# Kernel optimization log

Measured on AMD Instinct MI355X. Metric: run time of the kernel, lower is better.

Reference implementation:

```python
import jax, jax.numpy as jnp
import numpy as np

D_MODEL = 1024
N_HEADS = 16
SEQ = 2048
BATCH = 2
EPS = 1e-5


def layer_norm(x, g, b):
    mu = jnp.mean(x, axis=-1, keepdims=True)
    var = jnp.mean(jnp.square(x - mu), axis=-1, keepdims=True)
    return (x - mu) * jax.lax.rsqrt(var + EPS) * g + b


def setup_inputs() -> dict:
    key = jax.random.key(0)
    ks = jax.random.split(key, 10)
    D = D_MODEL
    s = lambda fan_in: 1.0 / np.sqrt(fan_in)
    return {
        "x": jax.random.normal(ks[0], (BATCH, SEQ, D), dtype=jnp.float32),
        # weights stored [in, out] (torch Linear is y = x @ W.T; equivalent math)
        "w_attn": jax.random.uniform(ks[1], (D, 3 * D), minval=-s(D), maxval=s(D), dtype=jnp.float32),
        "b_attn": jnp.zeros((3 * D,), jnp.float32),
        "w_proj": jax.random.uniform(ks[2], (D, D), minval=-s(D), maxval=s(D), dtype=jnp.float32),
        "b_proj": jnp.zeros((D,), jnp.float32),
        "ln1_g": jnp.ones((D,), jnp.float32),
        "ln1_b": jnp.zeros((D,), jnp.float32),
        "ln2_g": jnp.ones((D,), jnp.float32),
        "ln2_b": jnp.zeros((D,), jnp.float32),
        "w_fc1": jax.random.uniform(ks[3], (D, 4 * D), minval=-s(D), maxval=s(D), dtype=jnp.float32),
        "b_fc1": jnp.zeros((4 * D,), jnp.float32),
        "w_fc2": jax.random.uniform(ks[4], (4 * D, D), minval=-s(4 * D), maxval=s(4 * D), dtype=jnp.float32),
        "b_fc2": jnp.zeros((D,), jnp.float32),
    }


def reference(x, w_attn, b_attn, w_proj, b_proj, ln1_g, ln1_b, ln2_g, ln2_b, w_fc1, b_fc1, w_fc2, b_fc2):
    B, L, D = x.shape
    H = N_HEADS
    Dh = D // H

    # --- attention sublayer ---
    h = layer_norm(x, ln1_g, ln1_b)
    qkv = h @ w_attn + b_attn                      # [B, L, 3D]
    # SOURCE BUG (faithful): q, k, v are all taken from the k third.
    k = qkv[..., D:2 * D]
    kh = k.reshape(B, L, H, Dh).transpose(0, 2, 1, 3)   # [B, H, L, Dh]
    att = jnp.einsum('bhqd,bhkd->bhqk', kh, kh) / jnp.sqrt(jnp.float32(Dh))
    att = jax.nn.softmax(att, axis=-1)
    out = jnp.einsum('bhqk,bhkd->bhqd', att, kh)         # [B, H, L, Dh]
    out = out.transpose(0, 2, 1, 3).reshape(B, L, D)
    x = x + (out @ w_proj + b_proj)

    # --- feed-forward sublayer ---
    h = layer_norm(x, ln2_g, ln2_b)
    h = jax.nn.relu(h @ w_fc1 + b_fc1)
    x = x + (h @ w_fc2 + b_fc2)
    return x
```

## Files before the change

### kernel.cpp

```cpp
#include <hip/hip_runtime.h>


typedef __attribute__((ext_vector_type(8))) short s8v;
typedef __attribute__((ext_vector_type(4))) short s4v;
typedef __attribute__((ext_vector_type(4))) float f4v;

#define D_MODEL 1024
#define SEQ 2048
#define BATCH 2
#define NH 16
#define DH 64
#define MROWS (BATCH * SEQ)

#define KH_SCALE 0.42466088f
#define KH_ISCALE 2.3548200f

__device__ __forceinline__ float b2f(unsigned short u) {
  union { unsigned int i; float f; } v; v.i = ((unsigned int)u) << 16; return v.f;
}
__device__ __forceinline__ unsigned short f2b(float f) {
  unsigned int i = __builtin_bit_cast(unsigned int, f);
  unsigned int r = (i + 0x7fffu + ((i >> 16) & 1u)) >> 16;
  return (unsigned short)r;
}
__device__ __forceinline__ void async16(const void* g, void* l) {
  __builtin_amdgcn_global_load_lds(
      (const __attribute__((address_space(1))) unsigned int*)g,
      (__attribute__((address_space(3))) unsigned int*)l, 16, 0, 0);
}
__device__ __forceinline__ unsigned short cvt_b(float f) { return f2b(f); }
__device__ __forceinline__ unsigned short cvt_b(unsigned short u) { return u; }

__device__ __forceinline__ float xp2(float x) {
#if __has_builtin(__builtin_amdgcn_exp2f)
  return __builtin_amdgcn_exp2f(x);
#else
  return exp2f(x);
#endif
}

__device__ __forceinline__ s4v cvt4(float a, float b, float c, float d) {
  unsigned int lo, hi;
  asm("v_cvt_pk_bf16_f32 %0, %1, %2" : "=v"(lo) : "v"(a), "v"(b));
  asm("v_cvt_pk_bf16_f32 %0, %1, %2" : "=v"(hi) : "v"(c), "v"(d));
  union { unsigned long long u; s4v v; } u;
  u.u = ((unsigned long long)hi << 32) | (unsigned long long)lo;
  return u.v;
}

#if __has_builtin(__builtin_amdgcn_mfma_f32_16x16x16_bf16)
__device__ __forceinline__ f4v mfma16(s4v a, s4v b, f4v c) {
  return __builtin_amdgcn_mfma_f32_16x16x16_bf16(a, b, c, 0, 0, 0);
}
#elif __has_builtin(__builtin_amdgcn_mfma_f32_16x16x16bf16_1k)
__device__ __forceinline__ f4v mfma16(s4v a, s4v b, f4v c) {
  return __builtin_amdgcn_mfma_f32_16x16x16bf16_1k(a, b, c, 0, 0, 0);
}
#else
__device__ __forceinline__ f4v mfma16(s4v a, s4v b, f4v c) {
  s8v aa = {a[0], a[1], a[2], a[3], 0, 0, 0, 0};
  s8v bb = {b[0], b[1], b[2], b[3], 0, 0, 0, 0};
  return __builtin_amdgcn_mfma_f32_16x16x32_bf16(aa, bb, c, 0, 0, 0);
}
#endif

__global__ __launch_bounds__(256) void ln_kernel(
    const float* __restrict__ x, const float* __restrict__ g,
    const float* __restrict__ bb, unsigned short* __restrict__ out) {
  int row = blockIdx.x;
  int t = threadIdx.x;
  const float* xr = x + (size_t)row * D_MODEL;
  float v[4];
  float s = 0.f, s2 = 0.f;
#pragma unroll
  for (int i = 0; i < 4; ++i) {
    float f = xr[t + 256 * i];
    v[i] = f; s += f; s2 += f * f;
  }
#pragma unroll
  for (int off = 1; off < 64; off <<= 1) {
    s += __shfl_xor(s, off, 64);
    s2 += __shfl_xor(s2, off, 64);
  }
  __shared__ float red[8];
  if ((t & 63) == 0) { red[t >> 6] = s; red[4 + (t >> 6)] = s2; }
  __syncthreads();
  s = red[0] + red[1] + red[2] + red[3];
  s2 = red[4] + red[5] + red[6] + red[7];
  float mu = s * (1.f / D_MODEL);
  float var = s2 * (1.f / D_MODEL) - mu * mu;
  float rstd = rsqrtf(var + 1e-5f);
#pragma unroll
  for (int i = 0; i < 4; ++i) {
    int c = t + 256 * i;
    float h = (v[i] - mu) * rstd * g[c] + bb[c];
    out[(size_t)row * D_MODEL + c] = f2b(h);
  }
}

template <typename T>
__global__ __launch_bounds__(256) void transpose_b(
    const T* __restrict__ src, unsigned short* __restrict__ dst,
    int srcStride, int dstStride, long long srcBatch, long long dstBatch) {
  __shared__ unsigned short tile[64][65];
  const T* s = src + (size_t)blockIdx.z * srcBatch;
  unsigned short* d = dst + (size_t)blockIdx.z * dstBatch;
  int n0 = blockIdx.x * 64, k0 = blockIdx.y * 64;
  for (int i = threadIdx.x; i < 4096; i += 256) {
    int k = i >> 6, n = i & 63;
    tile[k][n] = cvt_b(s[(size_t)(k0 + k) * srcStride + n0 + n]);
  }
  __syncthreads();
  for (int i = threadIdx.x; i < 4096; i += 256) {
    int n = i >> 6, k = i & 63;
    d[(size_t)(n0 + n) * dstStride + k0 + k] = tile[k][n];
  }
}

template <int RES, bool RELU, bool KH, int OUTF, int BN>
__global__ __launch_bounds__(256) void gemm_bt(
    const unsigned short* __restrict__ A, const unsigned short* __restrict__ Bt,
    const float* __restrict__ bias, const float* __restrict__ res,
    void* __restrict__ out, int M, int N, int K) {
  constexpr int NT = BN / 32;
  __shared__ __align__(16) unsigned short lsA[128 * 64];
  __shared__ __align__(16) unsigned short lsB[BN * 64];
  int tid = threadIdx.x;
  int lane = tid & 63, w = tid >> 6, quad = lane >> 4, l16 = lane & 15;
  int m0 = blockIdx.y * 128, n0 = blockIdx.x * BN;
  int wm = (w >> 1) * 64, wn = (w & 1) * (BN / 2);
  f4v acc[4][NT] = {};
  for (int kt = 0; kt < K; kt += 64) {
#pragma unroll
    for (int i = 0; i < 4; ++i) {
      int cb = w * 256 + i * 64;
      int ci = cb + lane;
      int row = ci >> 3, c = ci & 7;
      int cs = c ^ (row & 7);
      async16(A + (size_t)(m0 + row) * K + kt + cs * 8, &lsA[cb * 8]);
    }
#pragma unroll
    for (int i = 0; i < BN / 32; ++i) {
      int cb = w * (BN * 2) + i * 64;
      int ci = cb + lane;
      int row = ci >> 3, c = ci & 7;
      int cs = c ^ (row & 7);
      async16(Bt + (size_t)(n0 + row) * K + kt + cs * 8, &lsB[cb * 8]);
    }
    __builtin_amdgcn_s_waitcnt(0x0f70);
    __syncthreads();
#pragma unroll
    for (int s = 0; s < 2; ++s) {
      s8v af[4], bf[NT];
#pragma unroll
      for (int t = 0; t < 4; ++t) {
        int am = wm + t * 16 + l16;
        int ac = (s * 4 + quad) ^ (am & 7);
        af[t] = *(const s8v*)(&lsA[am * 64 + ac * 8]);
      }
#pragma unroll
      for (int t = 0; t < NT; ++t) {
        int bn = wn + t * 16 + l16;
        int bc = (s * 4 + quad) ^ (bn & 7);
        bf[t] = *(const s8v*)(&lsB[bn * 64 + bc * 8]);
      }
#pragma unroll
      for (int ti = 0; ti < 4; ++ti)
#pragma unroll
        for (int tj = 0; tj < NT; ++tj)
          acc[ti][tj] = __builtin_amdgcn_mfma_f32_16x16x32_bf16(
              af[ti], bf[tj], acc[ti][tj], 0, 0, 0);
    }
    __syncthreads();
  }
#pragma unroll
  for (int tj = 0; tj < NT; ++tj) {
    int col = n0 + wn + tj * 16 + l16;
    float bv = bias[col];
#pragma unroll
    for (int ti = 0; ti < 4; ++ti) {
#pragma unroll
      for (int r = 0; r < 4; ++r) {
        int rowg = m0 + wm + ti * 16 + quad * 4 + r;
        float vv = acc[ti][tj][r] + bv;
        if (KH) vv *= KH_SCALE;
        if (RES == 2) vv += res[(size_t)rowg * N + col];
        if (RELU) vv = fmaxf(vv, 0.f);
        size_t oidx;
        if (KH) {
          int b = rowg >> 11, l = rowg & 2047, h = col >> 6, d = col & 63;
          oidx = (((size_t)(b * NH + h)) * SEQ + l) * DH + d;
        } else {
          oidx = (size_t)rowg * N + col;
        }
        if (OUTF == 0) ((unsigned short*)out)[oidx] = f2b(vv);
        else           ((float*)out)[oidx] = vv;
      }
    }
  }
}

__global__ __launch_bounds__(256) void flash_k(
    const unsigned short* __restrict__ kh, const unsigned short* __restrict__ khT,
    unsigned short* __restrict__ Opart, float* __restrict__ lpart) {
  __shared__ __align__(16) unsigned short lsK[128 * 64];
  __shared__ __align__(16) unsigned short lsKT[64 * 128];
  int tid = threadIdx.x;
  int lane = tid & 63, w = tid >> 6, quad = lane >> 4, l16 = lane & 15;
  int split = blockIdx.x, bh = blockIdx.y, qb = blockIdx.z;
  const unsigned short* khB = kh + (size_t)bh * SEQ * DH;
  const unsigned short* khTB = khT + (size_t)bh * DH * SEQ;
  unsigned short* Op = Opart + (size_t)split * MROWS * D_MODEL;
  float* lp = lpart + (size_t)split * BATCH * NH * SEQ;
  s8v aQ[2][2];
#pragma unroll
  for (int g = 0; g < 2; ++g) {
    int q = qb * 128 + w * 32 + g * 16 + l16;
#pragma unroll
    for (int s = 0; s < 2; ++s)
      aQ[g][s] = *(const s8v*)(khB + (size_t)q * DH + s * 32 + quad * 8);
  }
  const s4v vone = {(short)0x3F80, (short)0x3F80, (short)0x3F80, (short)0x3F80};
  f4v accO[2][4] = {};
  f4v accL[2] = {};

  for (int kt8 = 0; kt8 < 8; ++kt8) {
    int key0 = split * 1024 + kt8 * 128;
#pragma unroll
    for (int i = 0; i < 4; ++i) {
      int cb = w * 256 + i * 64;
      int ci = cb + lane;
      int row = ci >> 3, c = ci & 7;
      int cs = c ^ (row & 7);
      async16(khB + (size_t)(key0 + row) * DH + cs * 8, &lsK[cb * 8]);
    }
#pragma unroll
    for (int i = 0; i < 4; ++i) {
      int cb = w * 256 + i * 64;
      int ci = cb + lane;
      int row = ci >> 4, c = ci & 15;
      int cs = c ^ (row & 15);
      async16(khTB + (size_t)row * SEQ + key0 + cs * 8, &lsKT[cb * 8]);
    }
    __builtin_amdgcn_s_waitcnt(0x0f70);
    __syncthreads();
#pragma unroll
    for (int half = 0; half < 2; ++half) {
      f4v accST[2][4] = {};
#pragma unroll
      for (int s = 0; s < 2; ++s) {
#pragma unroll
        for (int tj = 0; tj < 4; ++tj) {
          int key = half * 64 + tj * 16 + l16;
          int c = (s * 4 + quad) ^ (key & 7);
          s8v kf = *(const s8v*)(&lsK[key * 64 + c * 8]);
#pragma unroll
          for (int g = 0; g < 2; ++g)
            accST[g][tj] = __builtin_amdgcn_mfma_f32_16x16x32_bf16(
                kf, aQ[g][s], accST[g][tj], 0, 0, 0);
        }
      }
#pragma unroll
      for (int tj = 0; tj < 4; ++tj) {
        s4v pf[2];
#pragma unroll
        for (int g = 0; g < 2; ++g) {
          float p0 = xp2(accST[g][tj][0]);
          float p1 = xp2(accST[g][tj][1]);
          float p2 = xp2(accST[g][tj][2]);
          float p3 = xp2(accST[g][tj][3]);
          pf[g] = cvt4(p0, p1, p2, p3);
          accL[g] = mfma16(pf[g], vone, accL[g]);
        }
#pragma unroll
        for (int db = 0; db < 4; ++db) {
          int d = db * 16 + l16;
          int ch = (half * 8 + tj * 2 + (quad >> 1)) ^ (d & 15);
          s4v vf = *(const s4v*)(&lsKT[d * 128 + ch * 8 + (quad & 1) * 4]);
#pragma unroll
          for (int g = 0; g < 2; ++g)
            accO[g][db] = mfma16(pf[g], vf, accO[g][db]);
        }
      }
    }
    __syncthreads();
  }
  int b = bh >> 4, h = bh & 15;
#pragma unroll
  for (int g = 0; g < 2; ++g) {
    if (l16 == 0) {
#pragma unroll
      for (int r = 0; r < 4; ++r) {
        int q = qb * 128 + w * 32 + g * 16 + quad * 4 + r;
        lp[(size_t)bh * SEQ + q] = accL[g][r];
      }
    }
#pragma unroll
    for (int r = 0; r < 4; ++r) {
      int l = qb * 128 + w * 32 + g * 16 + quad * 4 + r;
#pragma unroll
      for (int db = 0; db < 4; ++db) {
        int d = db * 16 + l16;
        Op[((size_t)(b * SEQ + l)) * D_MODEL + h * DH + d] = f2b(accO[g][db][r]);
      }
    }
  }
}

__global__ __launch_bounds__(256) void attn_combine(
    const unsigned short* __restrict__ Opart, const float* __restrict__ lpart,
    unsigned short* __restrict__ attn) {
  int row = blockIdx.x;
  int b = row >> 11, l = row & 2047;
  int c0 = threadIdx.x * 4;
  int h = c0 >> 6;
  size_t lidx = (size_t)(b * NH + h) * SEQ + l;
  float ls = lpart[lidx] + lpart[(size_t)BATCH * NH * SEQ + lidx];
  float inv = KH_ISCALE / ls;
  s4v o0 = *(const s4v*)(Opart + (size_t)row * D_MODEL + c0);
  s4v o1 = *(const s4v*)(Opart + (size_t)MROWS * D_MODEL +
                         (size_t)row * D_MODEL + c0);
  s4v ov;
#pragma unroll
  for (int i = 0; i < 4; ++i)
    ov[i] = (short)f2b((b2f((unsigned short)o0[i]) +
                        b2f((unsigned short)o1[i])) * inv);
  *(s4v*)(attn + (size_t)row * D_MODEL + c0) = ov;
}

extern "C" void kernel_launch(void* const* d_in, const int* in_sizes, int n_in,
                              void* d_out, int out_size, void* d_ws, size_t ws_size,
                              hipStream_t stream) {
  (void)in_sizes; (void)n_in; (void)out_size;
  const float* x      = (const float*)d_in[0];
  const float* w_attn = (const float*)d_in[1];
  const float* b_attn = (const float*)d_in[2];
  const float* w_proj = (const float*)d_in[3];
  const float* b_proj = (const float*)d_in[4];
  const float* ln1_g  = (const float*)d_in[5];
  const float* ln1_b  = (const float*)d_in[6];
  const float* ln2_g  = (const float*)d_in[7];
  const float* ln2_b  = (const float*)d_in[8];
  const float* w_fc1  = (const float*)d_in[9];
  const float* b_fc1  = (const float*)d_in[10];
  const float* w_fc2  = (const float*)d_in[11];
  const float* b_fc2  = (const float*)d_in[12];

  char* ws = (char*)d_ws;
  float*          x1    = (float*)(ws);
  unsigned short* hbuf  = (unsigned short*)(ws + (size_t)(16u << 20));
  unsigned short* wT1   = (unsigned short*)(ws + (size_t)(24u << 20));
  unsigned short* wT2   = (unsigned short*)(ws + (size_t)(32u << 20));
  unsigned short* kh    = (unsigned short*)(ws + (size_t)(40u << 20));
  unsigned short* khT   = (unsigned short*)(ws + (size_t)(48u << 20));
  unsigned short* Opart = (unsigned short*)(ws);
  float*          lpart = (float*)(ws + (size_t)(16u << 20));
  unsigned short* fc1o  = kh;
  unsigned short* attn  = (unsigned short*)d_out;
  float* outf = (float*)d_out;
  bool big_ws = ws_size >= ((size_t)72u << 20);

  dim3 blk(256);
  hipLaunchKernelGGL(ln_kernel, dim3(MROWS), blk, 0, stream, x, ln1_g, ln1_b, hbuf);
  hipLaunchKernelGGL(transpose_b<float>, dim3(16, 16, 1), blk, 0, stream,
                     w_attn + 1024, wT1, 3 * D_MODEL, D_MODEL, 0LL, 0LL);
  hipLaunchKernelGGL((gemm_bt<0, false, true, 0, 64>), dim3(16, 32), blk, 0, stream,
                     hbuf, wT1, b_attn + 1024, nullptr, (void*)kh,
                     MROWS, D_MODEL, D_MODEL);
  hipLaunchKernelGGL(transpose_b<unsigned short>, dim3(1, 32, 32), blk, 0, stream,
                     kh, khT, DH, SEQ, (long long)(SEQ * DH), (long long)(DH * SEQ));
  hipLaunchKernelGGL(flash_k, dim3(2, 32, SEQ / 128), blk, 0, stream,
                     kh, khT, Opart, lpart);
  hipLaunchKernelGGL(attn_combine, dim3(MROWS), blk, 0, stream,
                     Opart, lpart, attn);
  hipLaunchKernelGGL(transpose_b<float>, dim3(16, 16, 1), blk, 0, stream,
                     w_proj, wT1, D_MODEL, D_MODEL, 0LL, 0LL);
  hipLaunchKernelGGL((gemm_bt<2, false, false, 1, 64>), dim3(16, 32), blk, 0, stream,
                     attn, wT1, b_proj, x, (void*)x1, MROWS, D_MODEL, D_MODEL);
  hipLaunchKernelGGL(ln_kernel, dim3(MROWS), blk, 0, stream, x1, ln2_g, ln2_b, hbuf);
  hipLaunchKernelGGL(transpose_b<float>, dim3(64, 16, 1), blk, 0, stream,
                     w_fc1, wT1, 4 * D_MODEL, D_MODEL, 0LL, 0LL);
  hipLaunchKernelGGL(transpose_b<float>, dim3(16, 64, 1), blk, 0, stream,
                     w_fc2, wT2, D_MODEL, 4 * D_MODEL, 0LL, 0LL);
  if (big_ws) {
    hipLaunchKernelGGL((gemm_bt<0, true, false, 0, 128>), dim3(32, 32), blk, 0, stream,
                       hbuf, wT1, b_fc1, nullptr, (void*)fc1o,
                       MROWS, 4 * D_MODEL, D_MODEL);
    hipLaunchKernelGGL((gemm_bt<2, false, false, 1, 64>), dim3(16, 32), blk, 0, stream,
                       fc1o, wT2, b_fc2, x1, (void*)outf,
                       MROWS, D_MODEL, 4 * D_MODEL);
  } else {
    for (int c = 0; c < 2; ++c) {
      const unsigned short* h2c = hbuf + (size_t)c * 2048 * D_MODEL;
      const float* x1c = x1 + (size_t)c * 2048 * D_MODEL;
      float* outc = outf + (size_t)c * 2048 * D_MODEL;
      hipLaunchKernelGGL((gemm_bt<0, true, false, 0, 128>), dim3(32, 16), blk, 0, stream,
                         h2c, wT1, b_fc1, nullptr, (void*)fc1o,
                         2048, 4 * D_MODEL, D_MODEL);
      hipLaunchKernelGGL((gemm_bt<2, false, false, 1, 64>), dim3(16, 16), blk, 0, stream,
                         fc1o, wT2, b_fc2, x1c, (void*)outc,
                         2048, D_MODEL, 4 * D_MODEL);
    }
  }
}
```

Measured before the change: 346.9 us.

## Double-buffer GEMM LDS tiles to overlap global loads with MFMA

The bf16 GEMM now keeps two LDS buffers for the A and B tiles. It issues the async loads for the next K tile before computing the current one, and waits on vmcnt so only the older loads must finish. This hides global-memory latency behind the MFMA work. The fc1 GEMM also switches from BN=128 to BN=64 with twice as many blocks, likely to keep LDS use and occupancy in check now that shared memory is doubled. The cost is more LDS per block and less register reuse per block for fc1.

```diff
diff --git a/kernel.cpp b/kernel.cpp
--- a/kernel.cpp
+++ b/kernel.cpp
@@ -123,21 +123,22 @@
     const float* __restrict__ bias, const float* __restrict__ res,
     void* __restrict__ out, int M, int N, int K) {
   constexpr int NT = BN / 32;
-  __shared__ __align__(16) unsigned short lsA[128 * 64];
-  __shared__ __align__(16) unsigned short lsB[BN * 64];
+  __shared__ __align__(16) unsigned short lsA[2][128 * 64];
+  __shared__ __align__(16) unsigned short lsB[2][BN * 64];
   int tid = threadIdx.x;
   int lane = tid & 63, w = tid >> 6, quad = lane >> 4, l16 = lane & 15;
   int m0 = blockIdx.y * 128, n0 = blockIdx.x * BN;
   int wm = (w >> 1) * 64, wn = (w & 1) * (BN / 2);
   f4v acc[4][NT] = {};
-  for (int kt = 0; kt < K; kt += 64) {
+
+  auto stage = [&](int bsel, int ktE) {
 #pragma unroll
     for (int i = 0; i < 4; ++i) {
       int cb = w * 256 + i * 64;
       int ci = cb + lane;
       int row = ci >> 3, c = ci & 7;
       int cs = c ^ (row & 7);
-      async16(A + (size_t)(m0 + row) * K + kt + cs * 8, &lsA[cb * 8]);
+      async16(A + (size_t)(m0 + row) * K + ktE + cs * 8, &lsA[bsel][cb * 8]);
     }
 #pragma unroll
     for (int i = 0; i < BN / 32; ++i) {
@@ -145,10 +146,24 @@
       int ci = cb + lane;
       int row = ci >> 3, c = ci & 7;
       int cs = c ^ (row & 7);
-      async16(Bt + (size_t)(n0 + row) * K + kt + cs * 8, &lsB[cb * 8]);
-    }
-    __builtin_amdgcn_s_waitcnt(0x0f70);
-    __syncthreads();
+      async16(Bt + (size_t)(n0 + row) * K + ktE + cs * 8, &lsB[bsel][cb * 8]);
+    }
+  };
+
+  stage(0, 0);
+  int nK = K >> 6;
+  for (int kt = 0; kt < nK; ++kt) {
+    int b = kt & 1;
+    if (kt + 1 < nK) {
+      stage(b ^ 1, (kt + 1) << 6);
+      if constexpr (BN == 64) asm volatile("s_waitcnt vmcnt(6)" ::: "memory");
+      else                    asm volatile("s_waitcnt vmcnt(8)" ::: "memory");
+    } else {
+      asm volatile("s_waitcnt vmcnt(0)" ::: "memory");
+    }
+    __builtin_amdgcn_sched_barrier(0);
+    __builtin_amdgcn_s_barrier();
+    __builtin_amdgcn_sched_barrier(0);
 #pragma unroll
     for (int s = 0; s < 2; ++s) {
       s8v af[4], bf[NT];
@@ -156,13 +171,13 @@
       for (int t = 0; t < 4; ++t) {
         int am = wm + t * 16 + l16;
         int ac = (s * 4 + quad) ^ (am & 7);
-        af[t] = *(const s8v*)(&lsA[am * 64 + ac * 8]);
+        af[t] = *(const s8v*)(&lsA[b][am * 64 + ac * 8]);
       }
 #pragma unroll
       for (int t = 0; t < NT; ++t) {
         int bn = wn + t * 16 + l16;
         int bc = (s * 4 + quad) ^ (bn & 7);
-        bf[t] = *(const s8v*)(&lsB[bn * 64 + bc * 8]);
+        bf[t] = *(const s8v*)(&lsB[b][bn * 64 + bc * 8]);
       }
 #pragma unroll
       for (int ti = 0; ti < 4; ++ti)
@@ -171,7 +186,10 @@
           acc[ti][tj] = __builtin_amdgcn_mfma_f32_16x16x32_bf16(
               af[ti], bf[tj], acc[ti][tj], 0, 0, 0);
     }
-    __syncthreads();
+    asm volatile("s_waitcnt lgkmcnt(0)" ::: "memory");
+    __builtin_amdgcn_sched_barrier(0);
+    __builtin_amdgcn_s_barrier();
+    __builtin_amdgcn_sched_barrier(0);
   }
 #pragma unroll
   for (int tj = 0; tj < NT; ++tj) {
@@ -188,8 +206,8 @@
         if (RELU) vv = fmaxf(vv, 0.f);
         size_t oidx;
         if (KH) {
-          int b = rowg >> 11, l = rowg & 2047, h = col >> 6, d = col & 63;
-          oidx = (((size_t)(b * NH + h)) * SEQ + l) * DH + d;
+          int b2 = rowg >> 11, l = rowg & 2047, h = col >> 6, d = col & 63;
+          oidx = (((size_t)(b2 * NH + h)) * SEQ + l) * DH + d;
         } else {
           oidx = (size_t)rowg * N + col;
         }
@@ -383,7 +401,7 @@
   hipLaunchKernelGGL(transpose_b<float>, dim3(16, 64, 1), blk, 0, stream,
                      w_fc2, wT2, D_MODEL, 4 * D_MODEL, 0LL, 0LL);
   if (big_ws) {
-    hipLaunchKernelGGL((gemm_bt<0, true, false, 0, 128>), dim3(32, 32), blk, 0, stream,
+    hipLaunchKernelGGL((gemm_bt<0, true, false, 0, 64>), dim3(64, 32), blk, 0, stream,
                        hbuf, wT1, b_fc1, nullptr, (void*)fc1o,
                        MROWS, 4 * D_MODEL, D_MODEL);
     hipLaunchKernelGGL((gemm_bt<2, false, false, 1, 64>), dim3(16, 32), blk, 0, stream,
@@ -394,7 +412,7 @@
       const unsigned short* h2c = hbuf + (size_t)c * 2048 * D_MODEL;
       const float* x1c = x1 + (size_t)c * 2048 * D_MODEL;
       float* outc = outf + (size_t)c * 2048 * D_MODEL;
-      hipLaunchKernelGGL((gemm_bt<0, true, false, 0, 128>), dim3(32, 16), blk, 0, stream,
+      hipLaunchKernelGGL((gemm_bt<0, true, false, 0, 64>), dim3(64, 16), blk, 0, stream,
                          h2c, wT1, b_fc1, nullptr, (void*)fc1o,
                          2048, 4 * D_MODEL, D_MODEL);
       hipLaunchKernelGGL((gemm_bt<2, false, false, 1, 64>), dim3(16, 16), blk, 0, stream,
```

After: 347.2 us. Within noise of the previous version (+0.1%).
